# Kernel optimization log

Hardware: AMD Instinct MI355X
Metric: run time of the kernel (lower is better)

## Reference

```python
import jax, jax.numpy as jnp
import numpy as np

N = 131072      # H*W*batch = 128*128*8 features
D = 256         # feature_dim
P = 64          # proj_dim
E = 260096      # (2*H*W - H - W)*batch edges of the grid graph
G = 8192        # number of groups
SIM_THRESHOLD = 0.5


def setup_inputs() -> dict:
    key = jax.random.key(0)
    k0, k1, k2, k3 = jax.random.split(key, 4)
    features = jax.random.normal(k0, (N, D), dtype=jnp.float32)
    proj_W = jax.random.normal(k1, (D, P), dtype=jnp.float32) / np.sqrt(D)
    edge_index = jax.random.randint(k2, (2, E), 0, N, dtype=jnp.int64)
    group_ids = jax.random.randint(k3, (N,), 0, G, dtype=jnp.int64)
    return {
        "features": features,
        "proj_W": proj_W,
        "edge_index": edge_index,
        "group_ids": group_ids,
        "num_groups": G,
    }


def reference(features, proj_W, edge_index, group_ids, num_groups):
    # Projection: [N, D] @ [D, P] -> [N, P]
    proj = features @ proj_W
    # Pair comparison: gather both endpoints per edge, dot product per edge
    src, dst = edge_index[0], edge_index[1]
    sims = jnp.sum(proj[src] * proj[dst], axis=-1)            # [E]
    edge_logits = jax.nn.sigmoid(sims - SIM_THRESHOLD)        # [E]
    # Group mean pooling: scatter-add features per group, divide by size
    ones = jnp.ones((features.shape[0],), dtype=features.dtype)
    group_sums = jax.ops.segment_sum(features, group_ids, num_segments=num_groups)  # [G, D]
    group_sizes = jax.ops.segment_sum(ones, group_ids, num_segments=num_groups)     # [G]
    group_sizes = jnp.maximum(group_sizes, 1.0)
    group_means = group_sums / group_sizes[:, None]           # [G, D]
    return group_means, edge_logits
```

## Files before the change

kernel.cpp:

```cpp
#include <hip/hip_runtime.h>
#include <math.h>

constexpr int Nn = 131072;
constexpr int Dd = 256;
constexpr int Pp = 64;
constexpr int Gg = 8192;
constexpr int Ee = 260096;
constexpr int CAP = 64;
constexpr float SIM_TH = 0.5f;

typedef _Float16 half8 __attribute__((ext_vector_type(8)));
typedef _Float16 half4 __attribute__((ext_vector_type(4)));
typedef float floatx4 __attribute__((ext_vector_type(4)));


__global__ __launch_bounds__(256) void k_AB(
    const float* __restrict__ A,
    const float* __restrict__ W,
    _Float16* __restrict__ proj,
    const int* __restrict__ gid,
    int* __restrict__ cursor,
    int* __restrict__ bucket)
{
    if (blockIdx.x < 512) {
        const int i = blockIdx.x * 256 + threadIdx.x;
        const int g = gid[i];
        const int p = atomicAdd(&cursor[g], 1);
        if (p < CAP) bucket[g * CAP + p] = i;
        return;
    }

    __shared__ _Float16 WfL[16384];
    {
        const float4* __restrict__ W4 = reinterpret_cast<const float4*>(W);
#pragma unroll
        for (int u = 0; u < 16; ++u) {
            const int q4 = threadIdx.x + 256 * u;
            const float4 wv = W4[q4];
            const int m0 = q4 * 4;
#pragma unroll
            for (int e = 0; e < 4; ++e) {
                const int m = m0 + e;
                const int k = m >> 6;
                const int n = m & 63;
                const int i = ((k >> 5) << 11) + ((n >> 4) << 9)
                            + (((((k >> 3) & 3) << 4) + (n & 15)) << 3) + (k & 7);
                const float v = (e == 0) ? wv.x : (e == 1) ? wv.y
                              : (e == 2) ? wv.z : wv.w;
                WfL[i] = (_Float16)v;
            }
        }
    }
    __syncthreads();

    const int blk = blockIdx.x - 512;
    const int l = threadIdx.x & 63;
    const int w = threadIdx.x >> 6;
    const int rowbase = blk * 128 + w * 32;
    const int am = l & 15;
    const int q  = l >> 4;

    const float* __restrict__ a0p = A + (size_t)(rowbase + am) * Dd + q * 8;
    const float* __restrict__ a1p = a0p + 16 * Dd;
    const half8* __restrict__ bfrag = reinterpret_cast<const half8*>(WfL) + l;

    floatx4 acc0[4], acc1[4];
#pragma unroll
    for (int t = 0; t < 4; ++t) {
        acc0[t] = (floatx4){0.f, 0.f, 0.f, 0.f};
        acc1[t] = (floatx4){0.f, 0.f, 0.f, 0.f};
    }

#pragma unroll
    for (int c = 0; c < 8; ++c) {
        const float4 fa0 = *reinterpret_cast<const float4*>(a0p + c * 32);
        const float4 fb0 = *reinterpret_cast<const float4*>(a0p + c * 32 + 4);
        const float4 fa1 = *reinterpret_cast<const float4*>(a1p + c * 32);
        const float4 fb1 = *reinterpret_cast<const float4*>(a1p + c * 32 + 4);
        const half8 b0 = bfrag[(c * 4 + 0) * 64];
        const half8 b1 = bfrag[(c * 4 + 1) * 64];
        const half8 b2 = bfrag[(c * 4 + 2) * 64];
        const half8 b3 = bfrag[(c * 4 + 3) * 64];
        half8 a0, a1;
        a0[0] = (_Float16)fa0.x; a0[1] = (_Float16)fa0.y;
        a0[2] = (_Float16)fa0.z; a0[3] = (_Float16)fa0.w;
        a0[4] = (_Float16)fb0.x; a0[5] = (_Float16)fb0.y;
        a0[6] = (_Float16)fb0.z; a0[7] = (_Float16)fb0.w;
        a1[0] = (_Float16)fa1.x; a1[1] = (_Float16)fa1.y;
        a1[2] = (_Float16)fa1.z; a1[3] = (_Float16)fa1.w;
        a1[4] = (_Float16)fb1.x; a1[5] = (_Float16)fb1.y;
        a1[6] = (_Float16)fb1.z; a1[7] = (_Float16)fb1.w;
        acc0[0] = __builtin_amdgcn_mfma_f32_16x16x32_f16(a0, b0, acc0[0], 0, 0, 0);
        acc0[1] = __builtin_amdgcn_mfma_f32_16x16x32_f16(a0, b1, acc0[1], 0, 0, 0);
        acc0[2] = __builtin_amdgcn_mfma_f32_16x16x32_f16(a0, b2, acc0[2], 0, 0, 0);
        acc0[3] = __builtin_amdgcn_mfma_f32_16x16x32_f16(a0, b3, acc0[3], 0, 0, 0);
        acc1[0] = __builtin_amdgcn_mfma_f32_16x16x32_f16(a1, b0, acc1[0], 0, 0, 0);
        acc1[1] = __builtin_amdgcn_mfma_f32_16x16x32_f16(a1, b1, acc1[1], 0, 0, 0);
        acc1[2] = __builtin_amdgcn_mfma_f32_16x16x32_f16(a1, b2, acc1[2], 0, 0, 0);
        acc1[3] = __builtin_amdgcn_mfma_f32_16x16x32_f16(a1, b3, acc1[3], 0, 0, 0);
    }

#pragma unroll
    for (int r = 0; r < 4; ++r) {
        half4 h0, h1;
        h0[0] = (_Float16)acc0[0][r];
        h0[1] = (_Float16)acc0[1][r];
        h0[2] = (_Float16)acc0[2][r];
        h0[3] = (_Float16)acc0[3][r];
        h1[0] = (_Float16)acc1[0][r];
        h1[1] = (_Float16)acc1[1][r];
        h1[2] = (_Float16)acc1[2][r];
        h1[3] = (_Float16)acc1[3][r];
        *reinterpret_cast<half4*>(
            proj + (size_t)(rowbase + q * 4 + r) * Pp + am * 4) = h0;
        *reinterpret_cast<half4*>(
            proj + (size_t)(rowbase + 16 + q * 4 + r) * Pp + am * 4) = h1;
    }
}

__global__ __launch_bounds__(256) void k_CD(
    const float* __restrict__ features,
    const int* __restrict__ bucket,
    const int* __restrict__ cnt,
    float* __restrict__ out_means,
    const _Float16* __restrict__ proj,
    const int* __restrict__ ei,
    float* __restrict__ out_logits)
{
    if (blockIdx.x < 4096) {
        __shared__ float4 part[2][2][64];

        const int lane = threadIdx.x & 63;
        const int w    = threadIdx.x >> 6;
        const int gs   = w >> 1;
        const int half = w & 1;
        const int g = blockIdx.x * 2 + gs;
        const int n = min(cnt[g], CAP);
        const int col = lane * 4;
        const int* __restrict__ bk = bucket + g * CAP;

        float4 s = make_float4(0.f, 0.f, 0.f, 0.f);
        int k = half;
        for (; k + 14 < n; k += 16) {
            int r[8];
#pragma unroll
            for (int u = 0; u < 8; ++u) r[u] = bk[k + 2 * u];
            float4 f[8];
#pragma unroll
            for (int u = 0; u < 8; ++u)
                f[u] = *reinterpret_cast<const float4*>(features + (size_t)r[u] * Dd + col);
#pragma unroll
            for (int u = 0; u < 8; ++u) {
                s.x += f[u].x; s.y += f[u].y; s.z += f[u].z; s.w += f[u].w;
            }
        }
        for (; k < n; k += 2) {
            const float4 f = *reinterpret_cast<const float4*>(features + (size_t)bk[k] * Dd + col);
            s.x += f.x; s.y += f.y; s.z += f.z; s.w += f.w;
        }
        part[gs][half][lane] = s;
        __syncthreads();

        if (half == 0) {
            const float4 o = part[gs][1][lane];
            s.x += o.x; s.y += o.y; s.z += o.z; s.w += o.w;
            const float inv = 1.0f / (float)max(n, 1);
            s.x *= inv; s.y *= inv; s.z *= inv; s.w *= inv;
            *reinterpret_cast<float4*>(out_means + (size_t)g * Dd + col) = s;
        }
        return;
    }

    const int bid = blockIdx.x - 4096;
    const int sub = threadIdx.x & 7;
    const int sg  = bid * 32 + (threadIdx.x >> 3);
    const int e0  = sg * 4;

    int s[4], t[4];
#pragma unroll
    for (int u = 0; u < 4; ++u) { s[u] = ei[e0 + u]; t[u] = ei[Ee + e0 + u]; }

    half8 a[4], b[4];
#pragma unroll
    for (int u = 0; u < 4; ++u) {
        a[u] = *reinterpret_cast<const half8*>(proj + (size_t)s[u] * Pp + sub * 8);
        b[u] = *reinterpret_cast<const half8*>(proj + (size_t)t[u] * Pp + sub * 8);
    }

    float v[4];
#pragma unroll
    for (int u = 0; u < 4; ++u) {
        float acc = 0.f;
#pragma unroll
        for (int j = 0; j < 8; ++j)
            acc = fmaf((float)a[u][j], (float)b[u][j], acc);
        v[u] = acc;
    }

#pragma unroll
    for (int off = 4; off >= 1; off >>= 1) {
#pragma unroll
        for (int u = 0; u < 4; ++u) v[u] += __shfl_xor(v[u], off, 64);
    }

    if (sub < 4) {
        const float x = v[sub];
        out_logits[e0 + sub] = 1.0f / (1.0f + __expf(-(x - SIM_TH)));
    }
}

extern "C" void kernel_launch(void* const* d_in, const int* in_sizes, int n_in,
                              void* d_out, int out_size, void* d_ws, size_t ws_size,
                              hipStream_t stream)
{
    const float* features = (const float*)d_in[0];
    const float* W        = (const float*)d_in[1];
    const int*   ei       = (const int*)d_in[2];
    const int*   gid      = (const int*)d_in[3];

    float* out_means  = (float*)d_out;
    float* out_logits = out_means + (size_t)Gg * Dd;

    _Float16*  proj    = (_Float16*)d_ws;
    int*       bucket  = (int*)(proj + (size_t)Nn * Pp);
    int*       cursor  = bucket + Gg * CAP;

    hipMemsetAsync(cursor, 0, (size_t)Gg * sizeof(int), stream);

    hipLaunchKernelGGL(k_AB, dim3(512 + Nn / 128), dim3(256), 0, stream,
                       features, W, proj, gid, cursor, bucket);
    hipLaunchKernelGGL(k_CD, dim3(4096 + Ee / 128), dim3(256), 0, stream,
                       features, bucket, cursor, out_means,
                       proj, ei, out_logits);
}
```

Measured before the change: 241.9 us.

## Fold bucketing into GEMM blocks and coarsen pooling and edge work per block

The group-bucketing atomics now run in the first 128 threads of every projection block instead of in separate blocks. In the second kernel, each wave pools four whole groups on its own, taking member indices from a wave shuffle instead of splitting groups across two waves with a shared-memory reduce. Each edge block now handles four passes of edges, which cuts the grid from thousands of blocks to about a thousand. Outputs use nontemporal stores. The aim is to cut block-launch and synchronisation overhead, but having far fewer waves in flight may expose more gather latency.

```diff
diff --git a/kernel.cpp b/kernel.cpp
--- a/kernel.cpp
+++ b/kernel.cpp
@@ -22,12 +22,14 @@
     int* __restrict__ cursor,
     int* __restrict__ bucket)
 {
-    if (blockIdx.x < 512) {
-        const int i = blockIdx.x * 256 + threadIdx.x;
+    const int tid = threadIdx.x;
+    const int bid = blockIdx.x;
+
+    if (tid < 128) {
+        const int i = bid * 128 + tid;
         const int g = gid[i];
         const int p = atomicAdd(&cursor[g], 1);
         if (p < CAP) bucket[g * CAP + p] = i;
-        return;
     }
 
     __shared__ _Float16 WfL[16384];
@@ -35,7 +37,7 @@
         const float4* __restrict__ W4 = reinterpret_cast<const float4*>(W);
 #pragma unroll
         for (int u = 0; u < 16; ++u) {
-            const int q4 = threadIdx.x + 256 * u;
+            const int q4 = tid + 256 * u;
             const float4 wv = W4[q4];
             const int m0 = q4 * 4;
 #pragma unroll
@@ -53,10 +55,9 @@
     }
     __syncthreads();
 
-    const int blk = blockIdx.x - 512;
-    const int l = threadIdx.x & 63;
-    const int w = threadIdx.x >> 6;
-    const int rowbase = blk * 128 + w * 32;
+    const int l = tid & 63;
+    const int w = tid >> 6;
+    const int rowbase = bid * 128 + w * 32;
     const int am = l & 15;
     const int q  = l >> 4;
 
@@ -127,85 +128,94 @@
     const int* __restrict__ ei,
     float* __restrict__ out_logits)
 {
-    if (blockIdx.x < 4096) {
-        __shared__ float4 part[2][2][64];
-
-        const int lane = threadIdx.x & 63;
-        const int w    = threadIdx.x >> 6;
-        const int gs   = w >> 1;
-        const int half = w & 1;
-        const int g = blockIdx.x * 2 + gs;
-        const int n = min(cnt[g], CAP);
+    const int tid  = threadIdx.x;
+    const int lane = tid & 63;
+    const int w    = tid >> 6;
+
+    if (blockIdx.x < 512) {
         const int col = lane * 4;
-        const int* __restrict__ bk = bucket + g * CAP;
-
-        float4 s = make_float4(0.f, 0.f, 0.f, 0.f);
-        int k = half;
-        for (; k + 14 < n; k += 16) {
-            int r[8];
-#pragma unroll
-            for (int u = 0; u < 8; ++u) r[u] = bk[k + 2 * u];
-            float4 f[8];
-#pragma unroll
-            for (int u = 0; u < 8; ++u)
-                f[u] = *reinterpret_cast<const float4*>(features + (size_t)r[u] * Dd + col);
-#pragma unroll
-            for (int u = 0; u < 8; ++u) {
-                s.x += f[u].x; s.y += f[u].y; s.z += f[u].z; s.w += f[u].w;
+#pragma unroll
+        for (int s = 0; s < 4; ++s) {
+            const int g = blockIdx.x * 16 + w * 4 + s;
+            const int n = min(cnt[g], CAP);
+            const int* __restrict__ bk = bucket + g * CAP;
+            const int myidx = bk[lane];
+
+            float sx = 0.f, sy = 0.f, sz = 0.f, sw = 0.f;
+            int u = 0;
+            for (; u + 7 < n; u += 8) {
+                int r[8];
+#pragma unroll
+                for (int j = 0; j < 8; ++j) r[j] = __shfl(myidx, u + j, 64);
+                float4 f[8];
+#pragma unroll
+                for (int j = 0; j < 8; ++j)
+                    f[j] = *reinterpret_cast<const float4*>(
+                        features + (size_t)r[j] * Dd + col);
+#pragma unroll
+                for (int j = 0; j < 8; ++j) {
+                    sx += f[j].x; sy += f[j].y; sz += f[j].z; sw += f[j].w;
+                }
             }
-        }
-        for (; k < n; k += 2) {
-            const float4 f = *reinterpret_cast<const float4*>(features + (size_t)bk[k] * Dd + col);
-            s.x += f.x; s.y += f.y; s.z += f.z; s.w += f.w;
-        }
-        part[gs][half][lane] = s;
-        __syncthreads();
-
-        if (half == 0) {
-            const float4 o = part[gs][1][lane];
-            s.x += o.x; s.y += o.y; s.z += o.z; s.w += o.w;
+            for (; u < n; ++u) {
+                const int r = __shfl(myidx, u, 64);
+                const float4 f = *reinterpret_cast<const float4*>(
+                    features + (size_t)r * Dd + col);
+                sx += f.x; sy += f.y; sz += f.z; sw += f.w;
+            }
             const float inv = 1.0f / (float)max(n, 1);
-            s.x *= inv; s.y *= inv; s.z *= inv; s.w *= inv;
-            *reinterpret_cast<float4*>(out_means + (size_t)g * Dd + col) = s;
+            floatx4 o;
+            o[0] = sx * inv; o[1] = sy * inv; o[2] = sz * inv; o[3] = sw * inv;
+            __builtin_nontemporal_store(
+                o, reinterpret_cast<floatx4*>(out_means + (size_t)g * Dd + col));
         }
         return;
     }
 
-    const int bid = blockIdx.x - 4096;
-    const int sub = threadIdx.x & 7;
-    const int sg  = bid * 32 + (threadIdx.x >> 3);
-    const int e0  = sg * 4;
-
-    int s[4], t[4];
-#pragma unroll
-    for (int u = 0; u < 4; ++u) { s[u] = ei[e0 + u]; t[u] = ei[Ee + e0 + u]; }
-
-    half8 a[4], b[4];
-#pragma unroll
-    for (int u = 0; u < 4; ++u) {
-        a[u] = *reinterpret_cast<const half8*>(proj + (size_t)s[u] * Pp + sub * 8);
-        b[u] = *reinterpret_cast<const half8*>(proj + (size_t)t[u] * Pp + sub * 8);
-    }
-
-    float v[4];
-#pragma unroll
-    for (int u = 0; u < 4; ++u) {
-        float acc = 0.f;
-#pragma unroll
-        for (int j = 0; j < 8; ++j)
-            acc = fmaf((float)a[u][j], (float)b[u][j], acc);
-        v[u] = acc;
-    }
-
-#pragma unroll
-    for (int off = 4; off >= 1; off >>= 1) {
-#pragma unroll
-        for (int u = 0; u < 4; ++u) v[u] += __shfl_xor(v[u], off, 64);
-    }
-
-    if (sub < 4) {
-        const float x = v[sub];
-        out_logits[e0 + sub] = 1.0f / (1.0f + __expf(-(x - SIM_TH)));
+    const int bb  = blockIdx.x - 512;
+    const int sub = tid & 7;
+    const int sgl = tid >> 3;
+
+#pragma unroll
+    for (int pass = 0; pass < 4; ++pass) {
+        const int sg = (bb * 4 + pass) * 32 + sgl;
+        const int e0 = sg * 4;
+
+        int s4[4], t4[4];
+#pragma unroll
+        for (int u = 0; u < 4; ++u) {
+            s4[u] = ei[e0 + u];
+            t4[u] = ei[Ee + e0 + u];
+        }
+
+        half8 a[4], b[4];
+#pragma unroll
+        for (int u = 0; u < 4; ++u) {
+            a[u] = *reinterpret_cast<const half8*>(proj + (size_t)s4[u] * Pp + sub * 8);
+            b[u] = *reinterpret_cast<const half8*>(proj + (size_t)t4[u] * Pp + sub * 8);
+        }
+
+        float v[4];
+#pragma unroll
+        for (int u = 0; u < 4; ++u) {
+            float acc = 0.f;
+#pragma unroll
+            for (int j = 0; j < 8; ++j)
+                acc = fmaf((float)a[u][j], (float)b[u][j], acc);
+            v[u] = acc;
+        }
+
+#pragma unroll
+        for (int off = 4; off >= 1; off >>= 1) {
+#pragma unroll
+            for (int u = 0; u < 4; ++u) v[u] += __shfl_xor(v[u], off, 64);
+        }
+
+        if (sub < 4) {
+            const float x = v[sub];
+            __builtin_nontemporal_store(
+                1.0f / (1.0f + __expf(-(x - SIM_TH))), out_logits + e0 + sub);
+        }
     }
 }
 
@@ -225,11 +235,11 @@
     int*       bucket  = (int*)(proj + (size_t)Nn * Pp);
     int*       cursor  = bucket + Gg * CAP;
 
-    hipMemsetAsync(cursor, 0, (size_t)Gg * sizeof(int), stream);
-
-    hipLaunchKernelGGL(k_AB, dim3(512 + Nn / 128), dim3(256), 0, stream,
+    (void)hipMemsetAsync(cursor, 0, (size_t)Gg * sizeof(int), stream);
+
+    hipLaunchKernelGGL(k_AB, dim3(Nn / 128), dim3(256), 0, stream,
                        features, W, proj, gid, cursor, bucket);
-    hipLaunchKernelGGL(k_CD, dim3(4096 + Ee / 128), dim3(256), 0, stream,
+    hipLaunchKernelGGL(k_CD, dim3(512 + 508), dim3(256), 0, stream,
                        features, bucket, cursor, out_means,
                        proj, ei, out_logits);
 }
```

Result: no change. 244.6 us (+1.1%).
